# Performance work log

Measured on AMD Instinct MI355X. Metric: run time of the kernel, lower is better.

The kernel has to match this reference:

```python
import jax, jax.numpy as jnp
import numpy as np

B, C1, H, W = 2, 128, 64, 64
C_ = C1 // 2


def _conv2d(x, w, b, pad, dil):
    out = jax.lax.conv_general_dilated(
        x, w, (1, 1), [(pad, pad), (pad, pad)], rhs_dilation=(dil, dil),
        dimension_numbers=('NCHW', 'OIHW', 'NCHW'))
    return out + b[None, :, None, None]


def _deform_dw(x, off_w, off_b, w, k, pad, dil):
    # Depthwise DeformConv2d (v1, no modulation), offset_groups=1, stride=1.
    Bn, C, Hn, Wn = x.shape
    K = k * k
    offsets = _conv2d(x, off_w, off_b, pad, dil)          # [B, 2K, H, W]
    off = offsets.reshape(Bn, K, 2, Hn, Wn)               # (dy, dx) per kernel pt
    ky = jnp.repeat(jnp.arange(k) * dil, k).astype(x.dtype)   # [K]
    kx = jnp.tile(jnp.arange(k) * dil, k).astype(x.dtype)     # [K]
    py = off[:, :, 0] + (jnp.arange(Hn, dtype=x.dtype)[:, None] - pad) + ky[None, :, None, None]
    px = off[:, :, 1] + (jnp.arange(Wn, dtype=x.dtype)[None, :] - pad) + kx[None, :, None, None]
    y0 = jnp.floor(py); x0 = jnp.floor(px)
    ly = py - y0; lx = px - x0
    y0i = y0.astype(jnp.int32); x0i = x0.astype(jnp.int32)
    xf = x.reshape(Bn, C, Hn * Wn)

    def corner(yi, xi, wgt):
        valid = (yi >= 0) & (yi < Hn) & (xi >= 0) & (xi < Wn)
        idx = (jnp.clip(yi, 0, Hn - 1) * Wn + jnp.clip(xi, 0, Wn - 1)).reshape(Bn, -1)
        v = jax.vmap(lambda xb, ib: xb[:, ib])(xf, idx).reshape(Bn, C, K, Hn, Wn)
        return v * (wgt * valid.astype(x.dtype))[:, None]

    val = (corner(y0i, x0i, (1 - ly) * (1 - lx))
           + corner(y0i, x0i + 1, (1 - ly) * lx)
           + corner(y0i + 1, x0i, ly * (1 - lx))
           + corner(y0i + 1, x0i + 1, ly * lx))      # [B, C, K, H, W]
    return jnp.einsum('bckhw,ck->bchw', val, w.reshape(C, K))


def _forward(x, cv0_off_w, cv0_off_b, cv0_w, cvs_off_w, cvs_off_b, cvs_w,
             c0_off_w, c0_off_b, c0_w, cs_off_w, cs_off_b, cs_w,
             conv1_w, conv1_b, conv2_w, conv2_b):
    c = x.shape[1] // 2
    y0, y1 = x[:, :c], x[:, c:]
    a0 = _deform_dw(y0, cv0_off_w, cv0_off_b, cv0_w, 3, 1, 1)
    a0 = _deform_dw(a0, cvs_off_w, cvs_off_b, cvs_w, 5, 6, 3)
    a0 = _conv2d(a0, conv1_w, conv1_b, 0, 1)
    a1 = _deform_dw(y1, c0_off_w, c0_off_b, c0_w, 5, 2, 1)
    a1 = _deform_dw(a1, cs_off_w, cs_off_b, cs_w, 7, 9, 3)
    a1 = _conv2d(a1, conv2_w, conv2_b, 0, 1)
    return x * jnp.concatenate([a0, a1], axis=1)


def setup_inputs() -> dict:
    key = jax.random.key(0)
    ks = jax.random.split(key, 18)
    n = lambda k, sh, s: jax.random.normal(k, sh, dtype=jnp.float32) * s
    return {
        'x': n(ks[0], (B, C1, H, W), 1.0),
        'cv0_off_w': n(ks[1], (18, C_, 3, 3), 0.05),  'cv0_off_b': n(ks[2], (18,), 0.05),
        'cv0_w': n(ks[3], (C_, 1, 3, 3), 0.1),
        'cvs_off_w': n(ks[4], (50, C_, 5, 5), 0.05),  'cvs_off_b': n(ks[5], (50,), 0.05),
        'cvs_w': n(ks[6], (C_, 1, 5, 5), 0.1),
        'c0_off_w': n(ks[7], (50, C_, 5, 5), 0.05),   'c0_off_b': n(ks[8], (50,), 0.05),
        'c0_w': n(ks[9], (C_, 1, 5, 5), 0.1),
        'cs_off_w': n(ks[10], (98, C_, 7, 7), 0.05),  'cs_off_b': n(ks[11], (98,), 0.05),
        'cs_w': n(ks[12], (C_, 1, 7, 7), 0.1),
        'conv1_w': n(ks[13], (C_, C_, 1, 1), 0.1),    'conv1_b': n(ks[14], (C_,), 0.05),
        'conv2_w': n(ks[15], (C_, C_, 1, 1), 0.1),    'conv2_b': n(ks[16], (C_,), 0.05),
    }


def reference(x, cv0_off_w, cv0_off_b, cv0_w, cvs_off_w, cvs_off_b, cvs_w,
              c0_off_w, c0_off_b, c0_w, cs_off_w, cs_off_b, cs_w,
              conv1_w, conv1_b, conv2_w, conv2_b):
    return _forward(x, cv0_off_w, cv0_off_b, cv0_w, cvs_off_w, cvs_off_b, cvs_w,
                    c0_off_w, c0_off_b, c0_w, cs_off_w, cs_off_b, cs_w,
                    conv1_w, conv1_b, conv2_w, conv2_b)
```

## Files before the change

kernel.cpp:

```cpp
#include <hip/hip_runtime.h>
#include <hip/hip_bf16.h>

#define HW   4096

typedef __bf16 bf_t;
typedef __bf16 bf8_t __attribute__((ext_vector_type(8)));
typedef float  f4_t  __attribute__((ext_vector_type(4)));
typedef int    i4_t  __attribute__((ext_vector_type(4)));

#define OFF_A    0
#define OFF_B    409600
#define A1_F32   1212416
#define B1_F32   1736704
#define A2_F32   2260992
#define B2_F32   2785280
#define XA_F32   3309568
#define XB_F32   3833856
#define XA_HI    4358144
#define XA_LO    4620288
#define XB_HI    4882432
#define XB_LO    5144576
#define A1_HI    5406720
#define A1_LO    5668864
#define B1_HI    5931008
#define B1_LO    6193152
#define AW_A1    6455296
#define AW_B1    6464512
#define AW_A2    6515712
#define AW_B2    6566912
#define DW_A1    6767616
#define DW_B1    6768192
#define DW_A2    6769792
#define DW_B2    6771392
#define PRE_S1_A 6774528
#define PRE_S1_B 7364352
#define PRE_S2_A 6774528
#define PRE_S2_B 8412928
#define WS_TOT   11624192

__device__ __align__(16) float g_ws[WS_TOT];

__device__ __forceinline__ bf8_t bf8_zero() {
    bf8_t v;
#pragma unroll
    for (int j = 0; j < 8; ++j) v[j] = (bf_t)0.f;
    return v;
}

__device__ __forceinline__ void prep_wA_dev(const float* wg, int aw_off,
                                            int Cout, int K, int NCOT, int lb) {
    const int KK = K * K;
    const int total = KK * NCOT * 128;
    const int idx = lb * 256 + threadIdx.x;
    if (idx >= total) return;
    bf_t* aw = (bf_t*)(g_ws + aw_off);
    int lane = idx & 63;
    int kh   = (idx >> 6) & 1;
    int cot  = (idx >> 7) % NCOT;
    int tap  = idx / (128 * NCOT);
    int co   = cot * 16 + (lane & 15);
    int ci0  = kh * 32 + (lane >> 4) * 8;
    bf8_t v;
#pragma unroll
    for (int j = 0; j < 8; ++j) {
        float f = (co < Cout) ? wg[(co * 64 + ci0 + j) * KK + tap] : 0.f;
        v[j] = (bf_t)f;
    }
    *(bf8_t*)&aw[(long)idx * 8] = v;
}

__device__ __forceinline__ void prep_dwT_dev(const float* w, int dst_off,
                                             int KK, int lb) {
    const int idx = lb * 256 + threadIdx.x;
    if (idx < KK * 64) {
        int c = idx & 63, kk = idx >> 6;
        g_ws[dst_off + kk * 64 + c] = w[c * KK + kk];
    }
}

__global__ __launch_bounds__(256) void prep_all_kernel(
    const float* cv0_off_w, const float* c0_off_w,
    const float* cvs_off_w, const float* cs_off_w,
    const float* cv0_w, const float* c0_w,
    const float* cvs_w, const float* cs_w)
{
    const int bi = blockIdx.x;
    if      (bi < 9)   prep_wA_dev(cv0_off_w, AW_A1, 18, 3, 2, bi);
    else if (bi < 59)  prep_wA_dev(c0_off_w,  AW_B1, 50, 5, 4, bi - 9);
    else if (bi < 109) prep_wA_dev(cvs_off_w, AW_A2, 50, 5, 4, bi - 59);
    else if (bi < 305) prep_wA_dev(cs_off_w,  AW_B2, 98, 7, 8, bi - 109);
    else if (bi < 308) prep_dwT_dev(cv0_w, DW_A1, 9,  bi - 305);
    else if (bi < 315) prep_dwT_dev(c0_w,  DW_B1, 25, bi - 308);
    else if (bi < 322) prep_dwT_dev(cvs_w, DW_A2, 25, bi - 315);
    else               prep_dwT_dev(cs_w,  DW_B2, 49, bi - 322);
}

__global__ __launch_bounds__(256) void split_x_kernel(const float* __restrict__ x)
{
    const int bi = blockIdx.x;
    const int b  = bi & 1;
    const int br = bi >> 1;
    const float* sb = x + (long)b * (128 * HW) + (long)br * (64 * HW);
    bf_t*  dhi = (bf_t*)(g_ws + (br ? XB_HI : XA_HI));
    bf_t*  dlo = (bf_t*)(g_ws + (br ? XB_LO : XA_LO));
    float* df  = g_ws + (br ? XB_F32 : XA_F32);
    __shared__ float lds[16 * 68];
    const int p0 = blockIdx.y * 16;
    const int t  = threadIdx.x;
    {
        const int px = t & 15;
        const int c0 = t >> 4;
#pragma unroll
        for (int pass = 0; pass < 4; ++pass) {
            int ci = c0 + pass * 16;
            lds[px * 68 + ci] = sb[ci * HW + p0 + px];
        }
    }
    __syncthreads();
    if (t < 128) {
        int px = t >> 3, q = t & 7;
        bf8_t vh, vl;
        f4_t  f0, f1;
#pragma unroll
        for (int j = 0; j < 8; ++j) {
            float a = lds[px * 68 + q * 8 + j];
            bf_t hcast = (bf_t)a;
            vh[j] = hcast;
            vl[j] = (bf_t)(a - (float)hcast);
            if (j < 4) f0[j] = a; else f1[j - 4] = a;
        }
        long base = (((long)b * 4096 + p0 + px) * 64) + q * 8;
        *(bf8_t*)&dhi[base] = vh;
        *(bf8_t*)&dlo[base] = vl;
        *(f4_t*)&df[base]     = f0;
        *(f4_t*)&df[base + 4] = f1;
    }
}

template<int K, int DIL, int PAD, int NCOT, int CPG>
__global__ __launch_bounds__(256) void mfma_conv_kernel(
    int hi_off, int lo_off, int aw_off, const float* __restrict__ bias,
    int dst_off, int Cout)
{
    constexpr int COLS = 64 + 2 * PAD;
    const bf_t* shi = (const bf_t*)(g_ws + hi_off);
    const bf_t* slo = (const bf_t*)(g_ws + lo_off);
    const bf_t* aw  = (const bf_t*)(g_ws + aw_off);
    float* dst = g_ws + dst_off;
    __shared__ __align__(16) bf_t lds[2][COLS * 72];

    const int t    = threadIdx.x;
    const int lane = t & 63;
    const int wv   = t >> 6;
    const int b    = blockIdx.x >> 6;
    const int h    = blockIdx.x & 63;
    const int ct0  = blockIdx.y * CPG;

    const int n0 = lane & 15;
    const int kq = lane >> 4;

    f4_t acc[CPG];
#pragma unroll
    for (int i = 0; i < CPG; ++i) acc[i] = (f4_t){0.f, 0.f, 0.f, 0.f};

    for (int ky = 0; ky < K; ++ky) {
        const int ih = h - PAD + ky * DIL;
        __syncthreads();
        if ((unsigned)ih < 64u) {
            const long rowb = ((long)b * 4096 + ih * 64) * 64;
            for (int c = t; c < COLS * 8; c += 256) {
                int col = c >> 3, q = c & 7;
                int iw = col - PAD;
                bf8_t vh, vl;
                if ((unsigned)iw < 64u) {
                    vh = *(const bf8_t*)&shi[rowb + iw * 64 + q * 8];
                    vl = *(const bf8_t*)&slo[rowb + iw * 64 + q * 8];
                } else { vh = bf8_zero(); vl = bf8_zero(); }
                *(bf8_t*)&lds[0][col * 72 + q * 8] = vh;
                *(bf8_t*)&lds[1][col * 72 + q * 8] = vl;
            }
        } else {
            bf8_t z = bf8_zero();
            for (int c = t; c < COLS * 8; c += 256) {
                int col = c >> 3, q = c & 7;
                *(bf8_t*)&lds[0][col * 72 + q * 8] = z;
                *(bf8_t*)&lds[1][col * 72 + q * 8] = z;
            }
        }
        __syncthreads();
#pragma unroll
        for (int kx = 0; kx < K; ++kx) {
            const int tap = ky * K + kx;
            bf8_t afr[CPG][2];
#pragma unroll
            for (int ct = 0; ct < CPG; ++ct)
#pragma unroll
                for (int kh = 0; kh < 2; ++kh)
                    afr[ct][kh] = *(const bf8_t*)
                        &aw[((((long)tap * NCOT + ct0 + ct) * 2 + kh) * 64 + lane) * 8];
            const int colb = (wv * 16 + n0 + kx * DIL) * 72;
#pragma unroll
            for (int kh = 0; kh < 2; ++kh) {
                const bf8_t bh = *(const bf8_t*)&lds[0][colb + kh * 32 + kq * 8];
                const bf8_t bl = *(const bf8_t*)&lds[1][colb + kh * 32 + kq * 8];
#pragma unroll
                for (int ct = 0; ct < CPG; ++ct) {
                    acc[ct] = __builtin_amdgcn_mfma_f32_16x16x32_bf16(
                        afr[ct][kh], bh, acc[ct], 0, 0, 0);
                    acc[ct] = __builtin_amdgcn_mfma_f32_16x16x32_bf16(
                        afr[ct][kh], bl, acc[ct], 0, 0, 0);
                }
            }
        }
    }

    const int w = wv * 16 + n0;
#pragma unroll
    for (int ct = 0; ct < CPG; ++ct) {
#pragma unroll
        for (int r = 0; r < 4; ++r) {
            int co = (ct0 + ct) * 16 + kq * 4 + r;
            if (co < Cout)
                dst[((long)b * Cout + co) * HW + h * 64 + w] = acc[ct][r] + bias[co];
        }
    }
}

template<int K>
__device__ __forceinline__ void precomp_dev(int off_off, int pre_off,
                                            int pad, int dil, int lb) {
    constexpr int KK = K * K;
    const int idx = lb * 256 + threadIdx.x;
    const int p  = idx & 4095;
    const int r  = idx >> 12;
    const int kk = r % KK;
    const int b  = r / KK;
    const int h  = p >> 6, w = p & 63;

    const float oy = g_ws[off_off + ((long)(b * 2 * KK + 2 * kk)) * HW + p];
    const float ox = g_ws[off_off + ((long)(b * 2 * KK + 2 * kk + 1)) * HW + p];
    const float py = oy + (float)(h - pad + (kk / K) * dil);
    const float px = ox + (float)(w - pad + (kk % K) * dil);
    const float fy = floorf(py), fx = floorf(px);
    const float ly = py - fy,    lx = px - fx;
    const int y0 = (int)fy, x0 = (int)fx;
    const int y1 = y0 + 1,  x1 = x0 + 1;
    const float vy0 = ((unsigned)y0 < 64u) ? 1.f : 0.f;
    const float vy1 = ((unsigned)y1 < 64u) ? 1.f : 0.f;
    const float vx0 = ((unsigned)x0 < 64u) ? 1.f : 0.f;
    const float vx1 = ((unsigned)x1 < 64u) ? 1.f : 0.f;
    const float w00 = (1.f - ly) * (1.f - lx) * vy0 * vx0;
    const float w01 = (1.f - ly) * lx         * vy0 * vx1;
    const float w10 = ly         * (1.f - lx) * vy1 * vx0;
    const float w11 = ly         * lx         * vy1 * vx1;
    const int y0c = min(max(y0, 0), 63), y1c = min(max(y1, 0), 63);
    const int x0c = min(max(x0, 0), 63), x1c = min(max(x1, 0), 63);
    const int i00 = (y0c * 64 + x0c) * 256, i01 = (y0c * 64 + x1c) * 256;
    const int i10 = (y1c * 64 + x0c) * 256, i11 = (y1c * 64 + x1c) * 256;

    const long rb = (long)idx * 8;
    f4_t wv = {w00, w01, w10, w11};
    i4_t iv = {i00, i01, i10, i11};
    *(f4_t*)&g_ws[pre_off + rb]     = wv;
    *(i4_t*)&g_ws[pre_off + rb + 4] = iv;
}

template<int KA, int KB>
__global__ __launch_bounds__(256) void precomp_kernel(
    int offA, int preA, int padA, int dilA,
    int offB, int preB, int padB, int dilB, int blocksA)
{
    const int bi = blockIdx.x;
    if (bi < blocksA) precomp_dev<KA>(offA, preA, padA, dilA, bi);
    else              precomp_dev<KB>(offB, preB, padB, dilB, bi - blocksA);
}

template<int KK, int WRITE_HILO>
__device__ __forceinline__ void sample_dev(
    int bx, int src_off, int pre_off, int dwt_off,
    int dst_off, int hi_off, int lo_off)
{
    const int t  = threadIdx.x;
    const int c  = t & 63;
    const int pgi = ((bx & 7) << 8) | (bx >> 3);
    const int pg  = pgi * 4 + (t >> 6);
    const int b  = pg >> 12;
    const int p  = pg & 4095;

    const char* sb = (const char*)(g_ws + src_off + ((long)b << 18)) + (c << 2);
    const float* wtp = g_ws + dwt_off + c;
    int roff = (((b * KK) << 12) | p) * 8;
    roff = __builtin_amdgcn_readfirstlane(roff);
    const float* pre = g_ws + pre_off + roff;

    float acc = 0.f;
#pragma unroll 8
    for (int kk = 0; kk < KK; ++kk) {
        const float* rp = pre + kk * 32768;
        const f4_t wq = *(const f4_t*)rp;
        const i4_t iq = *(const i4_t*)(rp + 4);
        const float v00 = *(const float*)(sb + iq.x);
        const float v01 = *(const float*)(sb + iq.y);
        const float v10 = *(const float*)(sb + iq.z);
        const float v11 = *(const float*)(sb + iq.w);
        const float val = wq.x * v00 + wq.y * v01 + wq.z * v10 + wq.w * v11;
        acc = fmaf(wtp[kk * 64], val, acc);
    }

    const long ob = ((long)b * 4096 + p) * 64 + c;
    g_ws[dst_off + ob] = acc;
    if (WRITE_HILO) {
        bf_t h16 = (bf_t)acc;
        ((bf_t*)(g_ws + hi_off))[ob] = h16;
        ((bf_t*)(g_ws + lo_off))[ob] = (bf_t)(acc - (float)h16);
    }
}

template<int KKA, int KKB, int WRITE_HILO>
__global__ __launch_bounds__(256) void sample_kernel(
    int srcA, int preA, int dwtA, int dstA, int hiA, int loA,
    int srcB, int preB, int dwtB, int dstB, int hiB, int loB)
{
    const int bx = blockIdx.x;
    if (bx < 2048)
        sample_dev<KKA, WRITE_HILO>(bx, srcA, preA, dwtA, dstA, hiA, loA);
    else
        sample_dev<KKB, WRITE_HILO>(bx - 2048, srcB, preB, dwtB, dstB, hiB, loB);
}

__global__ __launch_bounds__(256) void final_kernel(
    const float* __restrict__ x,
    int aA_off, int aB_off,
    const float* __restrict__ w1, const float* __restrict__ b1,
    const float* __restrict__ w2, const float* __restrict__ b2,
    float* __restrict__ out)
{
    __shared__ float atile[64 * 65];
    __shared__ float wlds[64 * 32];
    const int t  = threadIdx.x;
    const int p0 = blockIdx.x * 64;
    const int by = blockIdx.y;
    const int b  = blockIdx.z;
    const bool brB  = (by >> 1) != 0;
    const int  cbase = (by & 1) * 32;
    const float* a  = g_ws + (brB ? aB_off : aA_off) + (long)b * (4096 * 64);
    const float* wg = brB ? w2 : w1;
    const float* bg = brB ? b2 : b1;

    {
        const int ci = t & 63;
        const int pxg = (t >> 6) * 16;
#pragma unroll
        for (int i = 0; i < 16; ++i) {
            int px = pxg + i;
            atile[px * 65 + ci] = a[(long)(p0 + px) * 64 + ci];
        }
    }
    for (int e = t; e < 2048; e += 256) {
        int col = e & 31, ci = e >> 5;
        wlds[ci * 32 + col] = wg[(cbase + col) * 64 + ci];
    }
    __syncthreads();

    const int px  = t & 63;
    const int cog = t >> 6;
    float acc[8] = {0, 0, 0, 0, 0, 0, 0, 0};
    for (int ci = 0; ci < 64; ++ci) {
        const float av = atile[px * 65 + ci];
        const float* wr = &wlds[ci * 32 + cog * 8];
#pragma unroll
        for (int j = 0; j < 8; ++j) acc[j] = fmaf(av, wr[j], acc[j]);
    }

    const int p = p0 + px;
#pragma unroll
    for (int j = 0; j < 8; ++j) {
        const int co = cbase + cog * 8 + j;
        const int cg = (brB ? 64 : 0) + co;
        const long o = ((long)b * 128 + cg) * HW + p;
        out[o] = (acc[j] + bg[co]) * x[o];
    }
}

extern "C" void kernel_launch(void* const* d_in, const int* in_sizes, int n_in,
                              void* d_out, int out_size, void* d_ws, size_t ws_size,
                              hipStream_t stream) {
    const float* x         = (const float*)d_in[0];
    const float* cv0_off_w = (const float*)d_in[1];
    const float* cv0_off_b = (const float*)d_in[2];
    const float* cv0_w     = (const float*)d_in[3];
    const float* cvs_off_w = (const float*)d_in[4];
    const float* cvs_off_b = (const float*)d_in[5];
    const float* cvs_w     = (const float*)d_in[6];
    const float* c0_off_w  = (const float*)d_in[7];
    const float* c0_off_b  = (const float*)d_in[8];
    const float* c0_w      = (const float*)d_in[9];
    const float* cs_off_w  = (const float*)d_in[10];
    const float* cs_off_b  = (const float*)d_in[11];
    const float* cs_w      = (const float*)d_in[12];
    const float* conv1_w   = (const float*)d_in[13];
    const float* conv1_b   = (const float*)d_in[14];
    const float* conv2_w   = (const float*)d_in[15];
    const float* conv2_b   = (const float*)d_in[16];
    float* out = (float*)d_out;
    (void)d_ws; (void)ws_size;

    prep_all_kernel<<<dim3(335), 256, 0, stream>>>(
        cv0_off_w, c0_off_w, cvs_off_w, cs_off_w, cv0_w, c0_w, cvs_w, cs_w);

    split_x_kernel<<<dim3(4, 256), 256, 0, stream>>>(x);

    mfma_conv_kernel<3, 1, 1, 2, 1><<<dim3(128, 2), 256, 0, stream>>>(
        XA_HI, XA_LO, AW_A1, cv0_off_b, OFF_A, 18);
    mfma_conv_kernel<5, 1, 2, 4, 1><<<dim3(128, 4), 256, 0, stream>>>(
        XB_HI, XB_LO, AW_B1, c0_off_b, OFF_B, 50);

    precomp_kernel<3, 5><<<dim3(1088), 256, 0, stream>>>(
        OFF_A, PRE_S1_A, 1, 1, OFF_B, PRE_S1_B, 2, 1, 288);

    sample_kernel<9, 25, 1><<<dim3(4096), 256, 0, stream>>>(
        XA_F32, PRE_S1_A, DW_A1, A1_F32, A1_HI, A1_LO,
        XB_F32, PRE_S1_B, DW_B1, B1_F32, B1_HI, B1_LO);

    mfma_conv_kernel<5, 3, 6, 4, 1><<<dim3(128, 4), 256, 0, stream>>>(
        A1_HI, A1_LO, AW_A2, cvs_off_b, OFF_A, 50);
    mfma_conv_kernel<7, 3, 9, 8, 2><<<dim3(128, 4), 256, 0, stream>>>(
        B1_HI, B1_LO, AW_B2, cs_off_b, OFF_B, 98);

    precomp_kernel<5, 7><<<dim3(2368), 256, 0, stream>>>(
        OFF_A, PRE_S2_A, 6, 3, OFF_B, PRE_S2_B, 9, 3, 800);

    sample_kernel<25, 49, 0><<<dim3(4096), 256, 0, stream>>>(
        A1_F32, PRE_S2_A, DW_A2, A2_F32, 0, 0,
        B1_F32, PRE_S2_B, DW_B2, B2_F32, 0, 0);

    final_kernel<<<dim3(64, 4, 2), 256, 0, stream>>>(
        x, A2_F32, B2_F32, conv1_w, conv1_b, conv2_w, conv2_b, out);
}
```

Baseline: 218.7 us.

## Fuse offset precompute into sampling and merge conv/prep launches

```diff
diff --git a/kernel.cpp b/kernel.cpp
--- a/kernel.cpp
+++ b/kernel.cpp
@@ -32,11 +32,7 @@
 #define DW_B1    6768192
 #define DW_A2    6769792
 #define DW_B2    6771392
-#define PRE_S1_A 6774528
-#define PRE_S1_B 7364352
-#define PRE_S2_A 6774528
-#define PRE_S2_B 8412928
-#define WS_TOT   11624192
+#define WS_TOT   6774528
 
 __device__ __align__(16) float g_ws[WS_TOT];
 
@@ -78,35 +74,35 @@
     }
 }
 
-__global__ __launch_bounds__(256) void prep_all_kernel(
+__global__ __launch_bounds__(256) void prep_split_kernel(
+    const float* __restrict__ x,
     const float* cv0_off_w, const float* c0_off_w,
     const float* cvs_off_w, const float* cs_off_w,
     const float* cv0_w, const float* c0_w,
     const float* cvs_w, const float* cs_w)
 {
+    __shared__ float lds[16 * 68];
     const int bi = blockIdx.x;
-    if      (bi < 9)   prep_wA_dev(cv0_off_w, AW_A1, 18, 3, 2, bi);
-    else if (bi < 59)  prep_wA_dev(c0_off_w,  AW_B1, 50, 5, 4, bi - 9);
-    else if (bi < 109) prep_wA_dev(cvs_off_w, AW_A2, 50, 5, 4, bi - 59);
-    else if (bi < 305) prep_wA_dev(cs_off_w,  AW_B2, 98, 7, 8, bi - 109);
-    else if (bi < 308) prep_dwT_dev(cv0_w, DW_A1, 9,  bi - 305);
-    else if (bi < 315) prep_dwT_dev(c0_w,  DW_B1, 25, bi - 308);
-    else if (bi < 322) prep_dwT_dev(cvs_w, DW_A2, 25, bi - 315);
-    else               prep_dwT_dev(cs_w,  DW_B2, 49, bi - 322);
-}
-
-__global__ __launch_bounds__(256) void split_x_kernel(const float* __restrict__ x)
-{
-    const int bi = blockIdx.x;
-    const int b  = bi & 1;
-    const int br = bi >> 1;
+    if (bi < 335) {
+        if      (bi < 9)   prep_wA_dev(cv0_off_w, AW_A1, 18, 3, 2, bi);
+        else if (bi < 59)  prep_wA_dev(c0_off_w,  AW_B1, 50, 5, 4, bi - 9);
+        else if (bi < 109) prep_wA_dev(cvs_off_w, AW_A2, 50, 5, 4, bi - 59);
+        else if (bi < 305) prep_wA_dev(cs_off_w,  AW_B2, 98, 7, 8, bi - 109);
+        else if (bi < 308) prep_dwT_dev(cv0_w, DW_A1, 9,  bi - 305);
+        else if (bi < 315) prep_dwT_dev(c0_w,  DW_B1, 25, bi - 308);
+        else if (bi < 322) prep_dwT_dev(cvs_w, DW_A2, 25, bi - 315);
+        else               prep_dwT_dev(cs_w,  DW_B2, 49, bi - 322);
+        return;
+    }
+    const int s  = bi - 335;
+    const int b  = s & 1;
+    const int br = (s >> 1) & 1;
+    const int p0 = (s >> 2) * 16;
     const float* sb = x + (long)b * (128 * HW) + (long)br * (64 * HW);
     bf_t*  dhi = (bf_t*)(g_ws + (br ? XB_HI : XA_HI));
     bf_t*  dlo = (bf_t*)(g_ws + (br ? XB_LO : XA_LO));
     float* df  = g_ws + (br ? XB_F32 : XA_F32);
-    __shared__ float lds[16 * 68];
-    const int p0 = blockIdx.y * 16;
-    const int t  = threadIdx.x;
+    const int t = threadIdx.x;
     {
         const int px = t & 15;
         const int c0 = t >> 4;
@@ -138,7 +134,8 @@
 }
 
 template<int K, int DIL, int PAD, int NCOT, int CPG>
-__global__ __launch_bounds__(256) void mfma_conv_kernel(
+__device__ __forceinline__ void mfma_conv_dev(
+    int bx, int by, bf_t* smem,
     int hi_off, int lo_off, int aw_off, const float* __restrict__ bias,
     int dst_off, int Cout)
 {
@@ -147,14 +144,15 @@
     const bf_t* slo = (const bf_t*)(g_ws + lo_off);
     const bf_t* aw  = (const bf_t*)(g_ws + aw_off);
     float* dst = g_ws + dst_off;
-    __shared__ __align__(16) bf_t lds[2][COLS * 72];
+    bf_t* lds0 = smem;
+    bf_t* lds1 = smem + COLS * 72;
 
     const int t    = threadIdx.x;
     const int lane = t & 63;
     const int wv   = t >> 6;
-    const int b    = blockIdx.x >> 6;
-    const int h    = blockIdx.x & 63;
-    const int ct0  = blockIdx.y * CPG;
+    const int b    = bx >> 6;
+    const int h    = bx & 63;
+    const int ct0  = by * CPG;
 
     const int n0 = lane & 15;
     const int kq = lane >> 4;
@@ -176,15 +174,15 @@
                     vh = *(const bf8_t*)&shi[rowb + iw * 64 + q * 8];
                     vl = *(const bf8_t*)&slo[rowb + iw * 64 + q * 8];
                 } else { vh = bf8_zero(); vl = bf8_zero(); }
-                *(bf8_t*)&lds[0][col * 72 + q * 8] = vh;
-                *(bf8_t*)&lds[1][col * 72 + q * 8] = vl;
+                *(bf8_t*)&lds0[col * 72 + q * 8] = vh;
+                *(bf8_t*)&lds1[col * 72 + q * 8] = vl;
             }
         } else {
             bf8_t z = bf8_zero();
             for (int c = t; c < COLS * 8; c += 256) {
                 int col = c >> 3, q = c & 7;
-                *(bf8_t*)&lds[0][col * 72 + q * 8] = z;
-                *(bf8_t*)&lds[1][col * 72 + q * 8] = z;
+                *(bf8_t*)&lds0[col * 72 + q * 8] = z;
+                *(bf8_t*)&lds1[col * 72 + q * 8] = z;
             }
         }
         __syncthreads();
@@ -201,8 +199,8 @@
             const int colb = (wv * 16 + n0 + kx * DIL) * 72;
 #pragma unroll
             for (int kh = 0; kh < 2; ++kh) {
-                const bf8_t bh = *(const bf8_t*)&lds[0][colb + kh * 32 + kq * 8];
-                const bf8_t bl = *(const bf8_t*)&lds[1][colb + kh * 32 + kq * 8];
+                const bf8_t bh = *(const bf8_t*)&lds0[colb + kh * 32 + kq * 8];
+                const bf8_t bl = *(const bf8_t*)&lds1[colb + kh * 32 + kq * 8];
 #pragma unroll
                 for (int ct = 0; ct < CPG; ++ct) {
                     acc[ct] = __builtin_amdgcn_mfma_f32_16x16x32_bf16(
@@ -226,77 +224,90 @@
     }
 }
 
-template<int K>
-__device__ __forceinline__ void precomp_dev(int off_off, int pre_off,
-                                            int pad, int dil, int lb) {
-    constexpr int KK = K * K;
-    const int idx = lb * 256 + threadIdx.x;
-    const int p  = idx & 4095;
-    const int r  = idx >> 12;
-    const int kk = r % KK;
-    const int b  = r / KK;
-    const int h  = p >> 6, w = p & 63;
-
-    const float oy = g_ws[off_off + ((long)(b * 2 * KK + 2 * kk)) * HW + p];
-    const float ox = g_ws[off_off + ((long)(b * 2 * KK + 2 * kk + 1)) * HW + p];
-    const float py = oy + (float)(h - pad + (kk / K) * dil);
-    const float px = ox + (float)(w - pad + (kk % K) * dil);
-    const float fy = floorf(py), fx = floorf(px);
-    const float ly = py - fy,    lx = px - fx;
-    const int y0 = (int)fy, x0 = (int)fx;
-    const int y1 = y0 + 1,  x1 = x0 + 1;
-    const float vy0 = ((unsigned)y0 < 64u) ? 1.f : 0.f;
-    const float vy1 = ((unsigned)y1 < 64u) ? 1.f : 0.f;
-    const float vx0 = ((unsigned)x0 < 64u) ? 1.f : 0.f;
-    const float vx1 = ((unsigned)x1 < 64u) ? 1.f : 0.f;
-    const float w00 = (1.f - ly) * (1.f - lx) * vy0 * vx0;
-    const float w01 = (1.f - ly) * lx         * vy0 * vx1;
-    const float w10 = ly         * (1.f - lx) * vy1 * vx0;
-    const float w11 = ly         * lx         * vy1 * vx1;
-    const int y0c = min(max(y0, 0), 63), y1c = min(max(y1, 0), 63);
-    const int x0c = min(max(x0, 0), 63), x1c = min(max(x1, 0), 63);
-    const int i00 = (y0c * 64 + x0c) * 256, i01 = (y0c * 64 + x1c) * 256;
-    const int i10 = (y1c * 64 + x0c) * 256, i11 = (y1c * 64 + x1c) * 256;
-
-    const long rb = (long)idx * 8;
-    f4_t wv = {w00, w01, w10, w11};
-    i4_t iv = {i00, i01, i10, i11};
-    *(f4_t*)&g_ws[pre_off + rb]     = wv;
-    *(i4_t*)&g_ws[pre_off + rb + 4] = iv;
-}
-
-template<int KA, int KB>
-__global__ __launch_bounds__(256) void precomp_kernel(
-    int offA, int preA, int padA, int dilA,
-    int offB, int preB, int padB, int dilB, int blocksA)
-{
+__global__ __launch_bounds__(256) void conv_s1_kernel(
+    const float* __restrict__ biasA, const float* __restrict__ biasB)
+{
+    extern __shared__ __align__(16) bf_t smem1[];
     const int bi = blockIdx.x;
-    if (bi < blocksA) precomp_dev<KA>(offA, preA, padA, dilA, bi);
-    else              precomp_dev<KB>(offB, preB, padB, dilB, bi - blocksA);
+    if (bi < 256)
+        mfma_conv_dev<3, 1, 1, 2, 1>(bi & 127, bi >> 7, smem1,
+                                     XA_HI, XA_LO, AW_A1, biasA, OFF_A, 18);
+    else {
+        const int s = bi - 256;
+        mfma_conv_dev<5, 1, 2, 4, 1>(s & 127, s >> 7, smem1,
+                                     XB_HI, XB_LO, AW_B1, biasB, OFF_B, 50);
+    }
+}
+
+__global__ __launch_bounds__(256) void conv_s2_kernel(
+    const float* __restrict__ biasA, const float* __restrict__ biasB)
+{
+    extern __shared__ __align__(16) bf_t smem2[];
+    const int bi = blockIdx.x;
+    if (bi < 512)
+        mfma_conv_dev<5, 3, 6, 4, 1>(bi & 127, bi >> 7, smem2,
+                                     A1_HI, A1_LO, AW_A2, biasA, OFF_A, 50);
+    else {
+        const int s = bi - 512;
+        mfma_conv_dev<7, 3, 9, 8, 2>(s & 127, s >> 7, smem2,
+                                     B1_HI, B1_LO, AW_B2, biasB, OFF_B, 98);
+    }
 }
 
 template<int KK, int WRITE_HILO>
-__device__ __forceinline__ void sample_dev(
-    int bx, int src_off, int pre_off, int dwt_off,
-    int dst_off, int hi_off, int lo_off)
-{
-    const int t  = threadIdx.x;
+__device__ __forceinline__ void sample_fused_dev(
+    int bx, float* recs, int src_off, int off_off, int dwt_off,
+    int dst_off, int hi_off, int lo_off, int K, int pad, int dil)
+{
+    const int t   = threadIdx.x;
+    const int pgi = ((bx & 7) << 8) | (bx >> 3);
+
+    for (int rec = t; rec < 4 * KK; rec += 256) {
+        const int wv = rec & 3;
+        const int kk = rec >> 2;
+        const int pg = pgi * 4 + wv;
+        const int b  = pg >> 12;
+        const int p  = pg & 4095;
+        const int h  = p >> 6, w = p & 63;
+        const float oy = g_ws[off_off + ((long)(b * 2 * KK + 2 * kk)) * HW + p];
+        const float ox = g_ws[off_off + ((long)(b * 2 * KK + 2 * kk + 1)) * HW + p];
+        const float py = oy + (float)(h - pad + (kk / K) * dil);
+        const float px = ox + (float)(w - pad + (kk % K) * dil);
+        const float fy = floorf(py), fx = floorf(px);
+        const float ly = py - fy,    lx = px - fx;
+        const int y0 = (int)fy, x0 = (int)fx;
+        const int y1 = y0 + 1,  x1 = x0 + 1;
+        const float vy0 = ((unsigned)y0 < 64u) ? 1.f : 0.f;
+        const float vy1 = ((unsigned)y1 < 64u) ? 1.f : 0.f;
+        const float vx0 = ((unsigned)x0 < 64u) ? 1.f : 0.f;
+        const float vx1 = ((unsigned)x1 < 64u) ? 1.f : 0.f;
+        const float w00 = (1.f - ly) * (1.f - lx) * vy0 * vx0;
+        const float w01 = (1.f - ly) * lx         * vy0 * vx1;
+        const float w10 = ly         * (1.f - lx) * vy1 * vx0;
+        const float w11 = ly         * lx         * vy1 * vx1;
+        const int y0c = min(max(y0, 0), 63), y1c = min(max(y1, 0), 63);
+        const int x0c = min(max(x0, 0), 63), x1c = min(max(x1, 0), 63);
+        const int i00 = (y0c * 64 + x0c) * 256, i01 = (y0c * 64 + x1c) * 256;
+        const int i10 = (y1c * 64 + x0c) * 256, i11 = (y1c * 64 + x1c) * 256;
+        float* rp = &recs[rec * 8];
+        *(f4_t*)rp       = (f4_t){w00, w01, w10, w11};
+        *(i4_t*)(rp + 4) = (i4_t){i00, i01, i10, i11};
+    }
+    __syncthreads();
+
     const int c  = t & 63;
-    const int pgi = ((bx & 7) << 8) | (bx >> 3);
-    const int pg  = pgi * 4 + (t >> 6);
+    const int wv = t >> 6;
+    const int pg = pgi * 4 + wv;
     const int b  = pg >> 12;
     const int p  = pg & 4095;
 
     const char* sb = (const char*)(g_ws + src_off + ((long)b << 18)) + (c << 2);
     const float* wtp = g_ws + dwt_off + c;
-    int roff = (((b * KK) << 12) | p) * 8;
-    roff = __builtin_amdgcn_readfirstlane(roff);
-    const float* pre = g_ws + pre_off + roff;
 
     float acc = 0.f;
 #pragma unroll 8
     for (int kk = 0; kk < KK; ++kk) {
-        const float* rp = pre + kk * 32768;
+        const float* rp = &recs[(kk * 4 + wv) * 8];
         const f4_t wq = *(const f4_t*)rp;
         const i4_t iq = *(const i4_t*)(rp + 4);
         const float v00 = *(const float*)(sb + iq.x);
@@ -316,16 +327,19 @@
     }
 }
 
-template<int KKA, int KKB, int WRITE_HILO>
+template<int KA, int KB, int WRITE_HILO>
 __global__ __launch_bounds__(256) void sample_kernel(
-    int srcA, int preA, int dwtA, int dstA, int hiA, int loA,
-    int srcB, int preB, int dwtB, int dstB, int hiB, int loB)
-{
+    int srcA, int offA, int dwtA, int dstA, int hiA, int loA, int padA, int dilA,
+    int srcB, int offB, int dwtB, int dstB, int hiB, int loB, int padB, int dilB)
+{
+    __shared__ __align__(16) float recs[4 * 49 * 8];
     const int bx = blockIdx.x;
     if (bx < 2048)
-        sample_dev<KKA, WRITE_HILO>(bx, srcA, preA, dwtA, dstA, hiA, loA);
+        sample_fused_dev<KA * KA, WRITE_HILO>(bx, recs, srcA, offA, dwtA,
+                                              dstA, hiA, loA, KA, padA, dilA);
     else
-        sample_dev<KKB, WRITE_HILO>(bx - 2048, srcB, preB, dwtB, dstB, hiB, loB);
+        sample_fused_dev<KB * KB, WRITE_HILO>(bx - 2048, recs, srcB, offB, dwtB,
+                                              dstB, hiB, loB, KB, padB, dilB);
 }
 
 __global__ __launch_bounds__(256) void final_kernel(
@@ -405,34 +419,20 @@
     float* out = (float*)d_out;
     (void)d_ws; (void)ws_size;
 
-    prep_all_kernel<<<dim3(335), 256, 0, stream>>>(
-        cv0_off_w, c0_off_w, cvs_off_w, cs_off_w, cv0_w, c0_w, cvs_w, cs_w);
-
-    split_x_kernel<<<dim3(4, 256), 256, 0, stream>>>(x);
-
-    mfma_conv_kernel<3, 1, 1, 2, 1><<<dim3(128, 2), 256, 0, stream>>>(
-        XA_HI, XA_LO, AW_A1, cv0_off_b, OFF_A, 18);
-    mfma_conv_kernel<5, 1, 2, 4, 1><<<dim3(128, 4), 256, 0, stream>>>(
-        XB_HI, XB_LO, AW_B1, c0_off_b, OFF_B, 50);
-
-    precomp_kernel<3, 5><<<dim3(1088), 256, 0, stream>>>(
-        OFF_A, PRE_S1_A, 1, 1, OFF_B, PRE_S1_B, 2, 1, 288);
-
-    sample_kernel<9, 25, 1><<<dim3(4096), 256, 0, stream>>>(
-        XA_F32, PRE_S1_A, DW_A1, A1_F32, A1_HI, A1_LO,
-        XB_F32, PRE_S1_B, DW_B1, B1_F32, B1_HI, B1_LO);
-
-    mfma_conv_kernel<5, 3, 6, 4, 1><<<dim3(128, 4), 256, 0, stream>>>(
-        A1_HI, A1_LO, AW_A2, cvs_off_b, OFF_A, 50);
-    mfma_conv_kernel<7, 3, 9, 8, 2><<<dim3(128, 4), 256, 0, stream>>>(
-        B1_HI, B1_LO, AW_B2, cs_off_b, OFF_B, 98);
-
-    precomp_kernel<5, 7><<<dim3(2368), 256, 0, stream>>>(
-        OFF_A, PRE_S2_A, 6, 3, OFF_B, PRE_S2_B, 9, 3, 800);
-
-    sample_kernel<25, 49, 0><<<dim3(4096), 256, 0, stream>>>(
-        A1_F32, PRE_S2_A, DW_A2, A2_F32, 0, 0,
-        B1_F32, PRE_S2_B, DW_B2, B2_F32, 0, 0);
+    prep_split_kernel<<<dim3(1359), 256, 0, stream>>>(
+        x, cv0_off_w, c0_off_w, cvs_off_w, cs_off_w, cv0_w, c0_w, cvs_w, cs_w);
+
+    conv_s1_kernel<<<dim3(768), 256, 19584, stream>>>(cv0_off_b, c0_off_b);
+
+    sample_kernel<3, 5, 1><<<dim3(4096), 256, 0, stream>>>(
+        XA_F32, OFF_A, DW_A1, A1_F32, A1_HI, A1_LO, 1, 1,
+        XB_F32, OFF_B, DW_B1, B1_F32, B1_HI, B1_LO, 2, 1);
+
+    conv_s2_kernel<<<dim3(1024), 256, 23616, stream>>>(cvs_off_b, cs_off_b);
+
+    sample_kernel<5, 7, 0><<<dim3(4096), 256, 0, stream>>>(
+        A1_F32, OFF_A, DW_A2, A2_F32, 0, 0, 6, 3,
+        B1_F32, OFF_B, DW_B2, B2_F32, 0, 0, 9, 3);
 
     final_kernel<<<dim3(64, 4, 2), 256, 0, stream>>>(
         x, A2_F32, B2_F32, conv1_w, conv1_b, conv2_w, conv2_b, out);
```

Result: faster. 201.1 us (median of 2 runs) (-8.0%).
